# Kernel tuning notes

Measured on AMD Instinct MI355X. Metric: run time of the kernel, lower is better.

## Reference

```python
import jax, jax.numpy as jnp
import numpy as np

PAD_IDX = 1
B, L, E, H = 2, 256, 512, 8
D = E // H
SCALE = D ** -0.5


def setup_inputs() -> dict:
    key = jax.random.key(0)
    ks = jax.random.split(key, 10)
    std = 0.02
    return {
        "queries": jax.random.normal(ks[0], (B, L, E), jnp.float32),
        "keys": jax.random.normal(ks[1], (B, L, E), jnp.float32),
        "values": jax.random.normal(ks[2], (B, L, E), jnp.float32),
        "relation": jax.random.normal(ks[3], (B, L, L, E), jnp.float32),
        "adj_mask": jax.random.randint(ks[4], (B, L, L), 0, 2, jnp.int32),
        "Wq": jax.random.normal(ks[5], (E, E), jnp.float32) * std,
        "bq": jnp.zeros((E,), jnp.float32),
        "Wk": jax.random.normal(ks[6], (E, E), jnp.float32) * std,
        "bk": jnp.zeros((E,), jnp.float32),
        "Wv": jax.random.normal(ks[7], (E, E), jnp.float32) * std,
        "bv": jnp.zeros((E,), jnp.float32),
        "Wr": jax.random.normal(ks[8], (2 * E, E), jnp.float32) * std,
        "Wo": jax.random.normal(ks[9], (E, E), jnp.float32) * std,
        "bo": jnp.zeros((E,), jnp.float32),
    }


def reference(queries, keys, values, relation, adj_mask,
              Wq, bq, Wk, bk, Wv, bv, Wr, Wo, bo):
    b, t, _ = queries.shape
    s = keys.shape[1]
    # input projections (torch Linear: y = x @ W.T + b)
    q = ((queries @ Wq.T + bq) * SCALE).reshape(b, t, H, D)
    k = (keys @ Wk.T + bk).reshape(b, s, H, D)
    v = (values @ Wv.T + bv).reshape(b, s, H, D)
    # relation projection -> relation queries/keys, [b, t, s, H, D] then transpose(1,2)
    rel = relation @ Wr.T                              # [b, t, s, 2E]
    rq, rk = jnp.split(rel, 2, axis=-1)
    rq = rq.reshape(b, t, s, H, D).transpose(0, 2, 1, 3, 4)  # [b, s, t, H, D]
    rk = rk.reshape(b, t, s, H, D).transpose(0, 2, 1, 3, 4)
    # broadcasted relation bias (requires t == s, as in the original)
    qe = q[:, :, None] + rq                            # [b, t, s, H, D]
    ke = k[:, None] + rk                               # [b, t, s, H, D]
    attn = jnp.einsum('bijhn,bijhn->bijh', qe, ke)     # [b, t, s, H]
    pad = (adj_mask == PAD_IDX)[..., None]             # [b, t, s, 1]
    attn = jnp.where(pad, -jnp.inf, attn)
    attn_weights = jax.nn.softmax(attn, axis=2)
    out = jnp.einsum('bijh,bjhn->bihn', attn_weights, v).reshape(b, t, E)
    out = out @ Wo.T + bo
    return out, attn_weights
```

## Files before the change

kernel.cpp:

```cpp
#include <hip/hip_runtime.h>

typedef unsigned int uint32;
typedef __attribute__((ext_vector_type(8))) short bf16x8;
typedef __attribute__((ext_vector_type(4))) float f32x4;


__device__ __forceinline__ uint32 bf_rne(uint32 u) {
  return (u + 0x7fffu + ((u >> 16) & 1u)) >> 16;
}

__global__ void cvt_wr_kernel(const float* __restrict__ Wr, unsigned short* __restrict__ WrBf) {
  int idx = blockIdx.x * 256 + threadIdx.x;
  const uint4* src = (const uint4*)Wr;
  uint4 x = src[idx];
  uint2 o;
  o.x = bf_rne(x.x) | (bf_rne(x.y) << 16);
  o.y = bf_rne(x.z) | (bf_rne(x.w) << 16);
  ((uint2*)WrBf)[idx] = o;
}

__global__ __launch_bounds__(256) void proj_kernel(
    const float* __restrict__ X0, const float* __restrict__ W0, const float* __restrict__ b0, float* __restrict__ Y0,
    const float* __restrict__ X1, const float* __restrict__ W1, const float* __restrict__ b1, float* __restrict__ Y1,
    const float* __restrict__ X2, const float* __restrict__ W2, const float* __restrict__ b2, float* __restrict__ Y2,
    float scale0) {
  int z = blockIdx.z;
  const float* X = (z == 0) ? X0 : (z == 1) ? X1 : X2;
  const float* W = (z == 0) ? W0 : (z == 1) ? W1 : W2;
  const float* bias = (z == 0) ? b0 : (z == 1) ? b1 : b2;
  float* Y = (z == 0) ? Y0 : (z == 1) ? Y1 : Y2;
  float scale = (z == 0) ? scale0 : 1.0f;

  __shared__ float Xs[16][68];
  __shared__ float Ws[16][68];

  int tid = threadIdx.x;
  int tx = tid & 15, ty = tid >> 4;
  int m0 = blockIdx.x * 64, n0 = blockIdx.y * 64;

  float acc[4][4] = {};

  for (int k0 = 0; k0 < 512; k0 += 16) {
#pragma unroll
    for (int u = 0; u < 4; ++u) {
      int idx = tid + u * 256;
      int ml = idx >> 4, kl = idx & 15;
      Xs[kl][ml] = X[(size_t)(m0 + ml) * 512 + k0 + kl];
      Ws[kl][ml] = W[(size_t)(n0 + ml) * 512 + k0 + kl];
    }
    __syncthreads();
#pragma unroll
    for (int kk = 0; kk < 16; ++kk) {
      float4 a = *(const float4*)&Xs[kk][ty * 4];
      float4 w = *(const float4*)&Ws[kk][tx * 4];
      float av[4] = {a.x, a.y, a.z, a.w};
      float wv[4] = {w.x, w.y, w.z, w.w};
#pragma unroll
      for (int i = 0; i < 4; ++i)
#pragma unroll
        for (int jj = 0; jj < 4; ++jj)
          acc[i][jj] += av[i] * wv[jj];
    }
    __syncthreads();
  }
#pragma unroll
  for (int i = 0; i < 4; ++i) {
    int m = m0 + ty * 4 + i;
#pragma unroll
    for (int jj = 0; jj < 4; ++jj) {
      int n = n0 + tx * 4 + jj;
      Y[(size_t)m * 512 + n] = (acc[i][jj] + bias[n]) * scale;
    }
  }
}

__global__ __launch_bounds__(512, 4) void rel_score_kernel(
    const float* __restrict__ rel,
    const unsigned short* __restrict__ wrbf,
    const float* __restrict__ qws,
    const float* __restrict__ kws,
    float* __restrict__ attn)
{
  __shared__ unsigned short As[64 * 512];
  __shared__ float scores[2][8][64];

  const int tid = threadIdx.x;
  const int lane = tid & 63;
  const int w = tid >> 6;
  const int wvl = w & 3;
  const int mt = blockIdx.x;
  const int b = mt >> 10;
  const int j = (mt >> 2) & 255;
  const int i0 = (mt & 3) << 6;

  const float* Abase = rel + (size_t)mt * (64 * 512);

  const int t15 = lane & 15;
  const int kq = (lane >> 4) * 8;
  const int rswz = (t15 & 7) << 3;

  const unsigned short* bptr[4];
#pragma unroll
  for (int fc = 0; fc < 4; ++fc) {
    int g = (wvl & 1) * 4 + fc;
    int head0 = (w >> 2) * 2 + (wvl >> 1);
    int wr_row = (g & 1) * 512 + head0 * 64 + (g >> 1) * 16 + t15;
    bptr[fc] = wrbf + (size_t)wr_row * 512 + kq;
  }

  const int arow = tid >> 3;
  const int ak8 = (tid & 7) * 8;
  const uint4* aq = (const uint4*)(Abase + (size_t)arow * 512 + ak8);
  const int wbase = arow * 512 + ak8;
  const int wswz = (arow & 7) << 3;

  f32x4 acc[4][4];

  auto epilogue = [&](int p) {
    const int head = (2 * p + (w >> 2)) * 2 + (wvl >> 1);
    const int dbase = (wvl & 1) * 32;
    const float* qbase = qws + ((size_t)(b * 256 + i0)) * 512 + head * 64;
    const float* krow = kws + ((size_t)(b * 256 + j)) * 512 + head * 64;
    const int rgrp = lane >> 4;
#pragma unroll
    for (int fr = 0; fr < 4; ++fr) {
#pragma unroll
      for (int r = 0; r < 4; ++r) {
        int m = fr * 16 + rgrp * 4 + r;
        float s = 0.f;
#pragma unroll
        for (int p2 = 0; p2 < 2; ++p2) {
          int d = dbase + p2 * 16 + t15;
          float qv = qbase[(size_t)m * 512 + d];
          float kv = krow[d];
          s += (qv + acc[fr][p2 * 2][r]) * (kv + acc[fr][p2 * 2 + 1][r]);
        }
        s += __shfl_xor(s, 1);
        s += __shfl_xor(s, 2);
        s += __shfl_xor(s, 4);
        s += __shfl_xor(s, 8);
        if (t15 == 0) scores[p][w][m] = s;
      }
    }
    __syncthreads();
    if (tid < 256) {
      int hl = tid >> 6, m = tid & 63;
      float sc = scores[p][hl * 2][m] + scores[p][hl * 2 + 1][m];
      attn[(((size_t)(b * 256 + i0 + m)) * 256 + j) * 8 + 4 * p + hl] = sc;
    }
  };

#pragma unroll
  for (int a = 0; a < 4; ++a)
#pragma unroll
    for (int c = 0; c < 4; ++c)
      acc[a][c] = (f32x4){0.f, 0.f, 0.f, 0.f};

  uint4 c0a = aq[0], c0b = aq[1];
  uint4 c1a = aq[16], c1b = aq[17];

#pragma unroll
  for (int k = 0; k < 8; ++k) {
    const int k0 = k * 64;
    bf16x8 bfr[2][4];
#pragma unroll
    for (int kh = 0; kh < 2; ++kh)
#pragma unroll
      for (int fc = 0; fc < 4; ++fc)
        bfr[kh][fc] = *(const bf16x8*)(bptr[fc] + k0 + kh * 32);
    {
      uint4 o;
      o.x = (c0a.y & 0xffff0000u) | (c0a.x >> 16);
      o.y = (c0a.w & 0xffff0000u) | (c0a.z >> 16);
      o.z = (c0b.y & 0xffff0000u) | (c0b.x >> 16);
      o.w = (c0b.w & 0xffff0000u) | (c0b.z >> 16);
      *(uint4*)&As[(wbase + k0) ^ wswz] = o;
    }
    c0a = c1a;
    c0b = c1b;
    if (k < 6) {
      c1a = aq[(k + 2) * 16];
      c1b = aq[(k + 2) * 16 + 1];
    }
    __syncthreads();
#pragma unroll
    for (int kh = 0; kh < 2; ++kh) {
      int kk = k0 + kh * 32 + kq;
      bf16x8 af[4];
#pragma unroll
      for (int fr = 0; fr < 4; ++fr)
        af[fr] = *(const bf16x8*)&As[((fr * 16 + t15) * 512 + kk) ^ rswz];
#pragma unroll
      for (int fr = 0; fr < 4; ++fr)
#pragma unroll
        for (int fc = 0; fc < 4; ++fc)
          acc[fr][fc] = __builtin_amdgcn_mfma_f32_16x16x32_bf16(
              af[fr], bfr[kh][fc], acc[fr][fc], 0, 0, 0);
    }
  }
  epilogue(0);

#pragma unroll
  for (int a = 0; a < 4; ++a)
#pragma unroll
    for (int c = 0; c < 4; ++c)
      acc[a][c] = (f32x4){0.f, 0.f, 0.f, 0.f};

  {
    const int hofs = 131072;

    bf16x8 bfr[2][4];
#pragma unroll
    for (int kh = 0; kh < 2; ++kh)
#pragma unroll
      for (int fc = 0; fc < 4; ++fc)
        bfr[kh][fc] = *(const bf16x8*)(bptr[fc] + hofs + kh * 32);

#pragma unroll
    for (int k = 0; k < 8; ++k) {
      const int k0 = k * 64;
      bf16x8 bnx[2][4];
      if (k < 7) {
#pragma unroll
        for (int kh = 0; kh < 2; ++kh)
#pragma unroll
          for (int fc = 0; fc < 4; ++fc)
            bnx[kh][fc] = *(const bf16x8*)(bptr[fc] + hofs + k0 + 64 + kh * 32);
      }
#pragma unroll
      for (int kh = 0; kh < 2; ++kh) {
        int kk = k0 + kh * 32 + kq;
        bf16x8 af[4];
#pragma unroll
        for (int fr = 0; fr < 4; ++fr)
          af[fr] = *(const bf16x8*)&As[((fr * 16 + t15) * 512 + kk) ^ rswz];
#pragma unroll
        for (int fr = 0; fr < 4; ++fr)
#pragma unroll
          for (int fc = 0; fc < 4; ++fc)
            acc[fr][fc] = __builtin_amdgcn_mfma_f32_16x16x32_bf16(
                af[fr], bfr[kh][fc], acc[fr][fc], 0, 0, 0);
      }
      if (k < 7) {
#pragma unroll
        for (int kh = 0; kh < 2; ++kh)
#pragma unroll
          for (int fc = 0; fc < 4; ++fc)
            bfr[kh][fc] = bnx[kh][fc];
      }
    }
  }
  epilogue(1);
}

__global__ __launch_bounds__(256) void softmax_av_kernel(
    float* __restrict__ attn, const int* __restrict__ adj,
    const float* __restrict__ vws, float* __restrict__ o1) {
  __shared__ float sl[2048];
  __shared__ int msk[256];
  int bi = blockIdx.x;
  int b = bi >> 8;
  float* base = attn + (size_t)bi * 2048;
  const int* abase = adj + (size_t)bi * 256;
  int tid = threadIdx.x;
#pragma unroll
  for (int u = 0; u < 8; ++u) sl[tid + u * 256] = base[tid + u * 256];
  msk[tid] = abase[tid];
  __syncthreads();
  int h = tid >> 5, l5 = tid & 31;
  float mx = -INFINITY;
#pragma unroll
  for (int u = 0; u < 8; ++u) {
    int jj = l5 + u * 32;
    if (msk[jj] != 1) mx = fmaxf(mx, sl[jj * 8 + h]);
  }
#pragma unroll
  for (int off = 16; off >= 1; off >>= 1) mx = fmaxf(mx, __shfl_xor(mx, off));
  float ev[8];
  float sum = 0.f;
#pragma unroll
  for (int u = 0; u < 8; ++u) {
    int jj = l5 + u * 32;
    float e = (msk[jj] != 1) ? __expf(sl[jj * 8 + h] - mx) : 0.f;
    ev[u] = e;
    sum += e;
  }
#pragma unroll
  for (int off = 16; off >= 1; off >>= 1) sum += __shfl_xor(sum, off);
  float inv = (sum > 0.f) ? (1.f / sum) : 0.f;
#pragma unroll
  for (int u = 0; u < 8; ++u) {
    int jj = l5 + u * 32;
    sl[jj * 8 + h] = ev[u] * inv;
  }
  __syncthreads();
#pragma unroll
  for (int u = 0; u < 8; ++u) base[tid + u * 256] = sl[tid + u * 256];
  const float* vbase = vws + (size_t)b * (256 * 512);
  int e0 = tid, e1 = tid + 256;
  int h0 = e0 >> 6, h1 = e1 >> 6;
  float a0 = 0.f, a1 = 0.f;
  for (int jj = 0; jj < 256; ++jj) {
    float w0 = sl[jj * 8 + h0];
    float w1 = sl[jj * 8 + h1];
    const float* vr = vbase + (size_t)jj * 512;
    a0 += w0 * vr[e0];
    a1 += w1 * vr[e1];
  }
  float* orow = o1 + (size_t)bi * 512;
  orow[e0] = a0;
  orow[e1] = a1;
}

extern "C" void kernel_launch(void* const* d_in, const int* in_sizes, int n_in,
                              void* d_out, int out_size, void* d_ws, size_t ws_size,
                              hipStream_t stream) {
  const float* queries = (const float*)d_in[0];
  const float* keys    = (const float*)d_in[1];
  const float* values  = (const float*)d_in[2];
  const float* relation = (const float*)d_in[3];
  const int*   adj     = (const int*)d_in[4];
  const float* Wq = (const float*)d_in[5];
  const float* bq = (const float*)d_in[6];
  const float* Wk = (const float*)d_in[7];
  const float* bk = (const float*)d_in[8];
  const float* Wv = (const float*)d_in[9];
  const float* bv = (const float*)d_in[10];
  const float* Wr = (const float*)d_in[11];
  const float* Wo = (const float*)d_in[12];
  const float* bo = (const float*)d_in[13];

  float* out  = (float*)d_out;
  float* attn = out + 262144;

  float* ws  = (float*)d_ws;
  float* qws = ws;
  float* kws = ws + 262144;
  float* vws = ws + 524288;
  float* o1  = ws + 786432;
  unsigned short* wrbf = (unsigned short*)(ws + 1048576);

  cvt_wr_kernel<<<dim3(512), dim3(256), 0, stream>>>(Wr, wrbf);

  proj_kernel<<<dim3(8, 8, 3), dim3(256), 0, stream>>>(
      queries, Wq, bq, qws,
      keys,    Wk, bk, kws,
      values,  Wv, bv, vws,
      0.125f);

  rel_score_kernel<<<dim3(2048), dim3(512), 0, stream>>>(relation, wrbf, qws, kws, attn);

  softmax_av_kernel<<<dim3(512), dim3(256), 0, stream>>>(attn, adj, vws, o1);

  proj_kernel<<<dim3(8, 8, 1), dim3(256), 0, stream>>>(
      o1, Wo, bo, out,
      nullptr, nullptr, nullptr, nullptr,
      nullptr, nullptr, nullptr, nullptr,
      1.0f);
}
```

Before: 818.0 us.

## Repartition rel_score waves over M halves and process heads in four passes

Each wave now owns half the 64 query rows and covers two heads per pass, with four passes over the head pairs instead of two passes of four heads. The accumulator array shrinks from 4x4 to 2x4 fragments, cutting register pressure, possibly allowing more occupancy. In exchange each wave reloads the shared A tile and the Wr fragments more times, adds two extra epilogues with their barriers, and the first K loop loses its deeper prefetch and full unrolling.

```diff
diff --git a/kernel.cpp b/kernel.cpp
--- a/kernel.cpp
+++ b/kernel.cpp
@@ -82,12 +82,15 @@
     float* __restrict__ attn)
 {
   __shared__ unsigned short As[64 * 512];
-  __shared__ float scores[2][8][64];
+  __shared__ float scores[2][2][2][64];
 
   const int tid = threadIdx.x;
   const int lane = tid & 63;
   const int w = tid >> 6;
-  const int wvl = w & 3;
+  const int mhalf = w >> 2;
+  const int nquad = w & 3;
+  const int head_sel = nquad >> 1;
+  const int dhalf = nquad & 1;
   const int mt = blockIdx.x;
   const int b = mt >> 10;
   const int j = (mt >> 2) & 255;
@@ -97,40 +100,36 @@
 
   const int t15 = lane & 15;
   const int kq = (lane >> 4) * 8;
+  const int rgrp = lane >> 4;
   const int rswz = (t15 & 7) << 3;
 
   const unsigned short* bptr[4];
 #pragma unroll
   for (int fc = 0; fc < 4; ++fc) {
-    int g = (wvl & 1) * 4 + fc;
-    int head0 = (w >> 2) * 2 + (wvl >> 1);
-    int wr_row = (g & 1) * 512 + head0 * 64 + (g >> 1) * 16 + t15;
+    int wr_row = (fc & 1) * 512 + head_sel * 64 + (dhalf * 2 + (fc >> 1)) * 16 + t15;
     bptr[fc] = wrbf + (size_t)wr_row * 512 + kq;
   }
 
   const int arow = tid >> 3;
-  const int ak8 = (tid & 7) * 8;
-  const uint4* aq = (const uint4*)(Abase + (size_t)arow * 512 + ak8);
-  const int wbase = arow * 512 + ak8;
+  const uint4* aq = (const uint4*)(Abase + (size_t)arow * 512 + (tid & 7) * 8);
+  const int wbase = arow * 512 + (tid & 7) * 8;
   const int wswz = (arow & 7) << 3;
 
-  f32x4 acc[4][4];
+  f32x4 acc[2][4];
 
   auto epilogue = [&](int p) {
-    const int head = (2 * p + (w >> 2)) * 2 + (wvl >> 1);
-    const int dbase = (wvl & 1) * 32;
+    const int head = 2 * p + head_sel;
     const float* qbase = qws + ((size_t)(b * 256 + i0)) * 512 + head * 64;
     const float* krow = kws + ((size_t)(b * 256 + j)) * 512 + head * 64;
-    const int rgrp = lane >> 4;
-#pragma unroll
-    for (int fr = 0; fr < 4; ++fr) {
+#pragma unroll
+    for (int fr = 0; fr < 2; ++fr) {
 #pragma unroll
       for (int r = 0; r < 4; ++r) {
-        int m = fr * 16 + rgrp * 4 + r;
+        int m = mhalf * 32 + fr * 16 + rgrp * 4 + r;
         float s = 0.f;
 #pragma unroll
         for (int p2 = 0; p2 < 2; ++p2) {
-          int d = dbase + p2 * 16 + t15;
+          int d = dhalf * 32 + p2 * 16 + t15;
           float qv = qbase[(size_t)m * 512 + d];
           float kv = krow[d];
           s += (qv + acc[fr][p2 * 2][r]) * (kv + acc[fr][p2 * 2 + 1][r]);
@@ -139,118 +138,103 @@
         s += __shfl_xor(s, 2);
         s += __shfl_xor(s, 4);
         s += __shfl_xor(s, 8);
-        if (t15 == 0) scores[p][w][m] = s;
+        if (t15 == 0) scores[p & 1][head_sel][dhalf][m] = s;
       }
     }
     __syncthreads();
-    if (tid < 256) {
-      int hl = tid >> 6, m = tid & 63;
-      float sc = scores[p][hl * 2][m] + scores[p][hl * 2 + 1][m];
-      attn[(((size_t)(b * 256 + i0 + m)) * 256 + j) * 8 + 4 * p + hl] = sc;
+    if (tid < 128) {
+      int hs = tid >> 6, m = tid & 63;
+      float sc = scores[p & 1][hs][0][m] + scores[p & 1][hs][1][m];
+      attn[(((size_t)(b * 256 + i0 + m)) * 256 + j) * 8 + 2 * p + hs] = sc;
     }
   };
 
 #pragma unroll
-  for (int a = 0; a < 4; ++a)
+  for (int a = 0; a < 2; ++a)
 #pragma unroll
     for (int c = 0; c < 4; ++c)
       acc[a][c] = (f32x4){0.f, 0.f, 0.f, 0.f};
 
-  uint4 c0a = aq[0], c0b = aq[1];
-  uint4 c1a = aq[16], c1b = aq[17];
-
-#pragma unroll
+  uint4 p0 = aq[0], p1 = aq[1];
+
   for (int k = 0; k < 8; ++k) {
     const int k0 = k * 64;
-    bf16x8 bfr[2][4];
-#pragma unroll
-    for (int kh = 0; kh < 2; ++kh)
-#pragma unroll
-      for (int fc = 0; fc < 4; ++fc)
-        bfr[kh][fc] = *(const bf16x8*)(bptr[fc] + k0 + kh * 32);
     {
       uint4 o;
-      o.x = (c0a.y & 0xffff0000u) | (c0a.x >> 16);
-      o.y = (c0a.w & 0xffff0000u) | (c0a.z >> 16);
-      o.z = (c0b.y & 0xffff0000u) | (c0b.x >> 16);
-      o.w = (c0b.w & 0xffff0000u) | (c0b.z >> 16);
+      o.x = (p0.y & 0xffff0000u) | (p0.x >> 16);
+      o.y = (p0.w & 0xffff0000u) | (p0.z >> 16);
+      o.z = (p1.y & 0xffff0000u) | (p1.x >> 16);
+      o.w = (p1.w & 0xffff0000u) | (p1.z >> 16);
       *(uint4*)&As[(wbase + k0) ^ wswz] = o;
     }
-    c0a = c1a;
-    c0b = c1b;
-    if (k < 6) {
-      c1a = aq[(k + 2) * 16];
-      c1b = aq[(k + 2) * 16 + 1];
+    if (k < 7) {
+      p0 = aq[(k + 1) * 16];
+      p1 = aq[(k + 1) * 16 + 1];
     }
     __syncthreads();
 #pragma unroll
     for (int kh = 0; kh < 2; ++kh) {
       int kk = k0 + kh * 32 + kq;
-      bf16x8 af[4];
-#pragma unroll
-      for (int fr = 0; fr < 4; ++fr)
-        af[fr] = *(const bf16x8*)&As[((fr * 16 + t15) * 512 + kk) ^ rswz];
-#pragma unroll
-      for (int fr = 0; fr < 4; ++fr)
+      bf16x8 bfr[4];
+#pragma unroll
+      for (int fc = 0; fc < 4; ++fc)
+        bfr[fc] = *(const bf16x8*)(bptr[fc] + k0 + kh * 32);
+      bf16x8 af[2];
+#pragma unroll
+      for (int fr = 0; fr < 2; ++fr)
+        af[fr] = *(const bf16x8*)&As[((mhalf * 32 + fr * 16 + t15) * 512 + kk) ^ rswz];
+#pragma unroll
+      for (int fr = 0; fr < 2; ++fr)
 #pragma unroll
         for (int fc = 0; fc < 4; ++fc)
           acc[fr][fc] = __builtin_amdgcn_mfma_f32_16x16x32_bf16(
-              af[fr], bfr[kh][fc], acc[fr][fc], 0, 0, 0);
+              af[fr], bfr[fc], acc[fr][fc], 0, 0, 0);
     }
   }
   epilogue(0);
 
-#pragma unroll
-  for (int a = 0; a < 4; ++a)
-#pragma unroll
-    for (int c = 0; c < 4; ++c)
-      acc[a][c] = (f32x4){0.f, 0.f, 0.f, 0.f};
-
-  {
-    const int hofs = 131072;
-
-    bf16x8 bfr[2][4];
-#pragma unroll
-    for (int kh = 0; kh < 2; ++kh)
-#pragma unroll
-      for (int fc = 0; fc < 4; ++fc)
-        bfr[kh][fc] = *(const bf16x8*)(bptr[fc] + hofs + kh * 32);
-
-#pragma unroll
-    for (int k = 0; k < 8; ++k) {
-      const int k0 = k * 64;
-      bf16x8 bnx[2][4];
-      if (k < 7) {
-#pragma unroll
-        for (int kh = 0; kh < 2; ++kh)
-#pragma unroll
-          for (int fc = 0; fc < 4; ++fc)
-            bnx[kh][fc] = *(const bf16x8*)(bptr[fc] + hofs + k0 + 64 + kh * 32);
+  for (int p = 1; p < 4; ++p) {
+#pragma unroll
+    for (int a = 0; a < 2; ++a)
+#pragma unroll
+      for (int c = 0; c < 4; ++c)
+        acc[a][c] = (f32x4){0.f, 0.f, 0.f, 0.f};
+
+    const int hofs = p * 65536;
+
+    bf16x8 bfr[4];
+#pragma unroll
+    for (int fc = 0; fc < 4; ++fc)
+      bfr[fc] = *(const bf16x8*)(bptr[fc] + hofs);
+
+#pragma unroll
+    for (int s = 0; s < 16; ++s) {
+      const int ks = s * 32;
+      bf16x8 bnx[4];
+      if (s < 15) {
+#pragma unroll
+        for (int fc = 0; fc < 4; ++fc)
+          bnx[fc] = *(const bf16x8*)(bptr[fc] + hofs + ks + 32);
       }
-#pragma unroll
-      for (int kh = 0; kh < 2; ++kh) {
-        int kk = k0 + kh * 32 + kq;
-        bf16x8 af[4];
-#pragma unroll
-        for (int fr = 0; fr < 4; ++fr)
-          af[fr] = *(const bf16x8*)&As[((fr * 16 + t15) * 512 + kk) ^ rswz];
-#pragma unroll
-        for (int fr = 0; fr < 4; ++fr)
-#pragma unroll
-          for (int fc = 0; fc < 4; ++fc)
-            acc[fr][fc] = __builtin_amdgcn_mfma_f32_16x16x32_bf16(
-                af[fr], bfr[kh][fc], acc[fr][fc], 0, 0, 0);
+      int kk = ks + kq;
+      bf16x8 af[2];
+#pragma unroll
+      for (int fr = 0; fr < 2; ++fr)
+        af[fr] = *(const bf16x8*)&As[((mhalf * 32 + fr * 16 + t15) * 512 + kk) ^ rswz];
+#pragma unroll
+      for (int fr = 0; fr < 2; ++fr)
+#pragma unroll
+        for (int fc = 0; fc < 4; ++fc)
+          acc[fr][fc] = __builtin_amdgcn_mfma_f32_16x16x32_bf16(
+              af[fr], bfr[fc], acc[fr][fc], 0, 0, 0);
+      if (s < 15) {
+#pragma unroll
+        for (int fc = 0; fc < 4; ++fc)
+          bfr[fc] = bnx[fc];
       }
-      if (k < 7) {
-#pragma unroll
-        for (int kh = 0; kh < 2; ++kh)
-#pragma unroll
-          for (int fc = 0; fc < 4; ++fc)
-            bfr[kh][fc] = bnx[kh][fc];
-      }
-    }
-  }
-  epilogue(1);
+    }
+    epilogue(p);
+  }
 }
 
 __global__ __launch_bounds__(256) void softmax_av_kernel(
```

Result: slower. 910.2 us (+11.3%).
